# Kernel tuning notes

Measured on AMD Instinct MI355X. Metric: run time of the kernel, lower is better.

## Reference

```python
import jax, jax.numpy as jnp
import numpy as np

N = 50000
E0 = 800000
IN_CH = 128
HID = 64
OUT_CH = 64
HEADS = 2
NEG_SLOPE = 0.2


def _xavier(key, shape):
    fan_in, fan_out = shape[-2], shape[-1]
    limit = (6.0 / (fan_in + fan_out)) ** 0.5
    return jax.random.uniform(key, shape, jnp.float32, -limit, limit)


def setup_inputs() -> dict:
    key = jax.random.key(0)
    ks = jax.random.split(key, 10)
    x = jax.random.normal(ks[0], (N, IN_CH), jnp.float32)
    src = jax.random.randint(ks[1], (E0,), 0, N)
    dst = jax.random.randint(ks[2], (E0,), 0, N)
    dst = jnp.where(src == dst, (dst + 1) % N, dst)  # no self loops in input
    edge_index = jnp.stack([src, dst]).astype(jnp.int64)
    emb_w = _xavier(ks[3], (HID, IN_CH))
    emb_b = jnp.zeros((HID,), jnp.float32)
    # layer 0: in=HID, out=HID, heads=HEADS
    w0 = _xavier(ks[4], (HEADS, HID, HID))
    a0 = _xavier(ks[5], (1, HEADS, 2 * HID))
    # layer 1: in=HEADS*HID, out=HID, heads=HEADS
    w1 = _xavier(ks[6], (HEADS, HEADS * HID, HID))
    a1 = _xavier(ks[7], (1, HEADS, 2 * HID))
    # layer 2: in=HEADS*HID, out=OUT_CH, heads=1, concat=False
    w2 = _xavier(ks[8], (1, HEADS * HID, OUT_CH))
    a2 = _xavier(ks[9], (1, 1, 2 * OUT_CH))
    return {"x": x, "edge_index": edge_index, "emb_w": emb_w, "emb_b": emb_b,
            "w0": w0, "a0": a0, "w1": w1, "a1": a1, "w2": w2, "a2": a2}


def gat_layer(x, w, a, src, dst, concat):
    # x: [N, F_in]; w: [H, F_in, C]; a: [1, H, 2C]; src/dst: [E]
    C = w.shape[-1]
    xh = jnp.einsum('nf,hfc->nhc', x, w)               # [N, H, C]
    a_i, a_j = a[0, :, :C], a[0, :, C:]                # each [H, C]
    # (cat(x_i, x_j) * a).sum(-1) == <x_i, a_i> + <x_j, a_j>; compute per node then gather
    s_i = jnp.einsum('nhc,hc->nh', xh, a_i)            # [N, H]
    s_j = jnp.einsum('nhc,hc->nh', xh, a_j)            # [N, H]
    alpha = jax.nn.leaky_relu(s_i[dst] + s_j[src], NEG_SLOPE)  # [E, H]
    # segment softmax over destination nodes
    m = jax.ops.segment_max(alpha, dst, num_segments=N)
    alpha = jnp.exp(alpha - m[dst])
    denom = jax.ops.segment_sum(alpha, dst, num_segments=N)
    alpha = alpha / (denom[dst] + 1e-16)
    out = jax.ops.segment_sum(xh[src] * alpha[:, :, None], dst, num_segments=N)  # [N, H, C]
    if concat:
        return out.reshape(N, -1)
    return out.mean(axis=1)


def _forward(x, edge_index, emb_w, emb_b, w0, a0, w1, a1, w2, a2):
    # add self loops (inputs contain none, matching remove+add in the source)
    loop = jnp.arange(N, dtype=edge_index.dtype)
    src = jnp.concatenate([edge_index[0], loop])
    dst = jnp.concatenate([edge_index[1], loop])
    h = x @ emb_w.T + emb_b                            # nn.Linear embedding
    h = jax.nn.elu(gat_layer(h, w0, a0, src, dst, True))
    h = jax.nn.elu(gat_layer(h, w1, a1, src, dst, True))
    h = jax.nn.elu(gat_layer(h, w2, a2, src, dst, False))
    return h


def reference(x, edge_index, emb_w, emb_b, w0, a0, w1, a1, w2, a2):
    return _forward(x, edge_index, emb_w, emb_b, w0, a0, w1, a1, w2, a2)
```

## Files before the change

### kernel.cpp

```cpp
#include <hip/hip_runtime.h>
#include <math.h>

typedef __attribute__((ext_vector_type(8))) short short8v;
typedef __attribute__((ext_vector_type(4))) float float4v;

union uf32 { unsigned int u; float f; };

__device__ __forceinline__ unsigned short f2b(float f) {
  uf32 v; v.f = f;
  unsigned int u = v.u;
  return (unsigned short)((u + 0x7fffu + ((u >> 16) & 1u)) >> 16);
}

__global__ void zero8(int* __restrict__ p, int n) {
  int i = blockIdx.x * 256 + threadIdx.x;
  if (i < n) p[i] = 0;
}

__global__ void hist8(const int* __restrict__ ei, int* __restrict__ cnt8,
                      unsigned short* __restrict__ lpos, int E0, int N) {
  int e = blockIdx.x * 256 + threadIdx.x;
  if (e >= E0 + N) return;
  int vx = blockIdx.x & 7;
  int d = (e < E0) ? ei[E0 + e] : (e - E0);
  lpos[e] = (unsigned short)atomicAdd(&cnt8[vx * N + d], 1);
}

__global__ void fold8(const int* __restrict__ cnt8, int* __restrict__ base8,
                      int* __restrict__ cnt, int* __restrict__ part, int N) {
  __shared__ int lds[256];
  int d = blockIdx.x * 256 + threadIdx.x;
  int run = 0;
  if (d < N) {
#pragma unroll
    for (int x = 0; x < 8; ++x) {
      int t = cnt8[x * N + d];
      base8[x * N + d] = run;
      run += t;
    }
    cnt[d] = run;
  }
  lds[threadIdx.x] = (d < N) ? run : 0;
  __syncthreads();
  for (int o = 128; o; o >>= 1) {
    if (threadIdx.x < o) lds[threadIdx.x] += lds[threadIdx.x + o];
    __syncthreads();
  }
  if (threadIdx.x == 0) part[blockIdx.x] = lds[0];
}

__global__ void scan_carry(int* __restrict__ part, int nb) {
  __shared__ int lds[256];
  __shared__ int carry;
  if (threadIdx.x == 0) carry = 0;
  __syncthreads();
  for (int t0 = 0; t0 < nb; t0 += 256) {
    int t = t0 + threadIdx.x;
    int v = (t < nb) ? part[t] : 0;
    lds[threadIdx.x] = v;
    __syncthreads();
    for (int o = 1; o < 256; o <<= 1) {
      int x = (threadIdx.x >= o) ? lds[threadIdx.x - o] : 0;
      __syncthreads();
      lds[threadIdx.x] += x;
      __syncthreads();
    }
    if (t < nb) part[t] = carry + lds[threadIdx.x] - v;
    __syncthreads();
    if (threadIdx.x == 255) carry += lds[255];
    __syncthreads();
  }
}

__global__ void scan3(const int* __restrict__ cnt, const int* __restrict__ part,
                      int* __restrict__ rp, int N, int E) {
  __shared__ int lds[256];
  int t = threadIdx.x;
  int idx = blockIdx.x * 256 + t;
  int v = (idx < N) ? cnt[idx] : 0;
  lds[t] = v;
  __syncthreads();
  for (int o = 1; o < 256; o <<= 1) {
    int x = (t >= o) ? lds[t - o] : 0;
    __syncthreads();
    lds[t] += x;
    __syncthreads();
  }
  if (idx < N) rp[idx] = part[blockIdx.x] + lds[t] - v;
  if (blockIdx.x == 0 && t == 0) rp[N] = E;
}

__global__ void addrp(const int* __restrict__ rp, const int* __restrict__ base8,
                      int* __restrict__ rb8, int N) {
  int d = blockIdx.x * 256 + threadIdx.x;
  int x = blockIdx.y;
  if (d < N) rb8[x * N + d] = rp[d] + base8[x * N + d];
}

__global__ void fillx(const int* __restrict__ ei, const int* __restrict__ rb8,
                      const unsigned short* __restrict__ lpos,
                      int* __restrict__ col, int E0, int N) {
  int e = blockIdx.x * 256 + threadIdx.x;
  if (e >= E0 + N) return;
  int vx = blockIdx.x & 7;
  int s, d;
  if (e < E0) { s = ei[e]; d = ei[E0 + e]; }
  else        { s = e - E0; d = s; }
  col[rb8[vx * N + d] + lpos[e]] = s;
}

__global__ void pack_w(const float* __restrict__ w, unsigned short* __restrict__ bp,
                       int F, int sf, int sc, int hstride) {
  int h = blockIdx.y;
  int i = blockIdx.x * 256 + threadIdx.x;
  if (i >= F * 64) return;
  int j = i & 7, colc = (i >> 3) & 15, g = (i >> 7) & 3, ct = (i >> 9) & 3, kk = i >> 11;
  int f = kk * 32 + g * 8 + j;
  int c = ct * 16 + colc;
  float v = w[(size_t)h * hstride + (size_t)f * sf + (size_t)c * sc];
  bp[(size_t)h * F * 64 + i] = f2b(v);
}

template <int F, int H, bool SCORES, bool BIAS, bool IBF, bool OBF>
__global__ __launch_bounds__(256) void gemm_mfma(
    const void* __restrict__ in, const unsigned short* __restrict__ bp,
    const float* __restrict__ bias, const float* __restrict__ a,
    void* __restrict__ xh_out, float* __restrict__ si, float* __restrict__ sj,
    int nrows) {
  constexpr int SA = F + 8;
  constexpr int NK = F / 32;
  constexpr int HC = H * 64;
  __shared__ __align__(16) unsigned short A_lds[64 * SA];

  const int tid = threadIdx.x;
  const int lane = tid & 63;
  const int wv = tid >> 6;
  const int h = blockIdx.y;
  const int n0 = blockIdx.x * 64;

  if (IBF) {
    const unsigned short* inb = (const unsigned short*)in;
    constexpr int NCH = 64 * F / 8;
#pragma unroll
    for (int i0 = 0; i0 < NCH; i0 += 256) {
      const int i = i0 + tid;
      const int row = i / (F / 8);
      const int c8 = i % (F / 8);
      int rg = n0 + row;
      if (rg >= nrows) rg = nrows - 1;
      const short8v v = *reinterpret_cast<const short8v*>(inb + (size_t)rg * F + c8 * 8);
      *reinterpret_cast<short8v*>(A_lds + row * SA + c8 * 8) = v;
    }
  } else {
    const float* inf = (const float*)in;
    constexpr int NCH = 64 * F / 4;
#pragma unroll
    for (int i0 = 0; i0 < NCH; i0 += 256) {
      const int i = i0 + tid;
      const int row = i / (F / 4);
      const int c4 = i % (F / 4);
      int rg = n0 + row;
      if (rg >= nrows) rg = nrows - 1;
      const float4 v = *reinterpret_cast<const float4*>(inf + (size_t)rg * F + c4 * 4);
      unsigned short* d = A_lds + row * SA + c4 * 4;
      d[0] = f2b(v.x); d[1] = f2b(v.y); d[2] = f2b(v.z); d[3] = f2b(v.w);
    }
  }
  __syncthreads();

  const int g = lane >> 4;
  const int cl = lane & 15;
  const unsigned short* __restrict__ bph = bp + (size_t)h * (NK * 4 * 4 * 128);

  float4v acc[4];
#pragma unroll
  for (int ct = 0; ct < 4; ++ct) acc[ct] = (float4v){0.f, 0.f, 0.f, 0.f};

  const unsigned short* ar = A_lds + (wv * 16 + cl) * SA + g * 8;
#pragma unroll
  for (int kk = 0; kk < NK; ++kk) {
    const short8v af = *reinterpret_cast<const short8v*>(ar + kk * 32);
#pragma unroll
    for (int ct = 0; ct < 4; ++ct) {
      const short8v bf = *reinterpret_cast<const short8v*>(
          bph + ((size_t)((kk * 4 + ct) * 4 + g)) * 128 + cl * 8);
      acc[ct] = __builtin_amdgcn_mfma_f32_16x16x32_bf16(af, bf, acc[ct], 0, 0, 0);
    }
  }

  if (BIAS) {
#pragma unroll
    for (int ct = 0; ct < 4; ++ct) {
      const float b = bias[ct * 16 + cl];
#pragma unroll
      for (int reg = 0; reg < 4; ++reg) acc[ct][reg] += b;
    }
  }

#pragma unroll
  for (int ct = 0; ct < 4; ++ct) {
    const int c = ct * 16 + cl;
#pragma unroll
    for (int reg = 0; reg < 4; ++reg) {
      const int n = n0 + wv * 16 + g * 4 + reg;
      if (n < nrows) {
        const size_t idx = (size_t)n * HC + h * 64 + c;
        if (OBF) ((unsigned short*)xh_out)[idx] = f2b(acc[ct][reg]);
        else     ((float*)xh_out)[idx] = acc[ct][reg];
      }
    }
  }

  if (SCORES) {
    float pi[4] = {0.f, 0.f, 0.f, 0.f}, pj[4] = {0.f, 0.f, 0.f, 0.f};
#pragma unroll
    for (int ct = 0; ct < 4; ++ct) {
      const float av = a[h * 128 + ct * 16 + cl];
      const float bv = a[h * 128 + 64 + ct * 16 + cl];
#pragma unroll
      for (int reg = 0; reg < 4; ++reg) {
        pi[reg] = fmaf(acc[ct][reg], av, pi[reg]);
        pj[reg] = fmaf(acc[ct][reg], bv, pj[reg]);
      }
    }
#pragma unroll
    for (int reg = 0; reg < 4; ++reg) {
#pragma unroll
      for (int o = 8; o; o >>= 1) {
        pi[reg] += __shfl_xor(pi[reg], o, 64);
        pj[reg] += __shfl_xor(pj[reg], o, 64);
      }
    }
    if (cl == 0) {
#pragma unroll
      for (int reg = 0; reg < 4; ++reg) {
        const int n = n0 + wv * 16 + g * 4 + reg;
        if (n < nrows) {
          si[(size_t)n * H + h] = pi[reg];
          sj[(size_t)n * H + h] = pj[reg];
        }
      }
    }
  }
}

template <int H, bool OBF>
__global__ __launch_bounds__(256) void agg_kernel(
    const unsigned short* __restrict__ xh, const float* __restrict__ si_g,
    const float* __restrict__ sj_g, const int* __restrict__ rp,
    const int* __restrict__ col, void* __restrict__ out, int N) {
  constexpr int HC = H * 64;
  const int lane = threadIdx.x & 63;
  const int n = blockIdx.x * 4 + (threadIdx.x >> 6);
  if (n >= N) return;
  const int el = lane & 31;
  const int hl = (H == 2) ? (lane >> 5) : 0;

  const int base = rp[n];
  const int deg = rp[n + 1] - base;
  const float siv = si_g[(size_t)n * H + hl];

  const int soff = (H == 1) ? (lane >> 5) : 0;
  const int qoff = (H == 1) ? (lane >> 5) : (lane & 32);
  constexpr int STEP = (H == 2) ? 1 : 2;
  const unsigned int loff = (H == 2) ? (unsigned)lane * 2 : (unsigned)el * 2;

  float m = -INFINITY, den = 0.f, acc0 = 0.f, acc1 = 0.f;

  for (int start = 0; start < deg; start += 32) {
    const int k = start + el;
    const bool vld = k < deg;
    const int s = vld ? col[base + k] : 0;
    float al = -INFINITY;
    if (vld) {
      const float t = siv + sj_g[(size_t)s * H + hl];
      al = (t > 0.f) ? t : 0.2f * t;
    }
    float cm = al;
#pragma unroll
    for (int o = 16; o; o >>= 1) cm = fmaxf(cm, __shfl_xor(cm, o, 64));
    const float nm = fmaxf(m, cm);
    const float r = __expf(m - nm);
    den *= r; acc0 *= r; acc1 *= r; m = nm;
    const float p = vld ? __expf(al - m) : 0.f;
    float ps = p;
#pragma unroll
    for (int o = 16; o; o >>= 1) ps += __shfl_xor(ps, o, 64);
    den += ps;

    const int cc = min(32, deg - start);
    int kk = 0;
    for (; kk + 4 * STEP <= cc; kk += 4 * STEP) {
      int sb[4]; float qb[4]; unsigned int uv[4];
#pragma unroll
      for (int u = 0; u < 4; ++u) {
        const int e = kk + u * STEP;
        sb[u] = __shfl(s, e + soff, 64);
        qb[u] = __shfl(p, e + qoff, 64);
      }
#pragma unroll
      for (int u = 0; u < 4; ++u)
        uv[u] = *reinterpret_cast<const unsigned int*>(xh + (size_t)sb[u] * HC + loff);
#pragma unroll
      for (int u = 0; u < 4; ++u) {
        uf32 lo, hi;
        lo.u = uv[u] << 16;
        hi.u = uv[u] & 0xffff0000u;
        acc0 = fmaf(qb[u], lo.f, acc0);
        acc1 = fmaf(qb[u], hi.f, acc1);
      }
    }
    for (; kk < cc; kk += STEP) {
      const int sb = __shfl(s, kk + soff, 64);
      const float qb = __shfl(p, kk + qoff, 64);
      const unsigned int uv = *reinterpret_cast<const unsigned int*>(xh + (size_t)sb * HC + loff);
      uf32 lo, hi;
      lo.u = uv << 16;
      hi.u = uv & 0xffff0000u;
      acc0 = fmaf(qb, lo.f, acc0);
      acc1 = fmaf(qb, hi.f, acc1);
    }
  }

  if (H == 2) {
    const float invd = 1.f / (den + 1e-16f);
    float v0 = acc0 * invd, v1 = acc1 * invd;
    v0 = (v0 > 0.f) ? v0 : expm1f(v0);
    v1 = (v1 > 0.f) ? v1 : expm1f(v1);
    if (OBF) {
      unsigned int pk = ((unsigned int)f2b(v1) << 16) | (unsigned int)f2b(v0);
      *reinterpret_cast<unsigned int*>((unsigned short*)out + (size_t)n * 128 + lane * 2) = pk;
    } else {
      float2 o; o.x = v0; o.y = v1;
      *reinterpret_cast<float2*>((float*)out + (size_t)n * 128 + lane * 2) = o;
    }
  } else {
    acc0 += __shfl_xor(acc0, 32, 64);
    acc1 += __shfl_xor(acc1, 32, 64);
    if (lane < 32) {
      const float invd = 1.f / (den + 1e-16f);
      float v0 = acc0 * invd, v1 = acc1 * invd;
      v0 = (v0 > 0.f) ? v0 : expm1f(v0);
      v1 = (v1 > 0.f) ? v1 : expm1f(v1);
      if (OBF) {
        unsigned int pk = ((unsigned int)f2b(v1) << 16) | (unsigned int)f2b(v0);
        *reinterpret_cast<unsigned int*>((unsigned short*)out + (size_t)n * 64 + el * 2) = pk;
      } else {
        float2 o; o.x = v0; o.y = v1;
        *reinterpret_cast<float2*>((float*)out + (size_t)n * 64 + el * 2) = o;
      }
    }
  }
}

extern "C" void kernel_launch(void* const* d_in, const int* in_sizes, int n_in,
                              void* d_out, int out_size, void* d_ws, size_t ws_size,
                              hipStream_t stream) {
  const float* x     = (const float*)d_in[0];
  const int*   ei    = (const int*)d_in[1];
  const float* emb_w = (const float*)d_in[2];
  const float* emb_b = (const float*)d_in[3];
  const float* w0    = (const float*)d_in[4];
  const float* a0    = (const float*)d_in[5];
  const float* w1    = (const float*)d_in[6];
  const float* a1    = (const float*)d_in[7];
  const float* w2    = (const float*)d_in[8];
  const float* a2    = (const float*)d_in[9];

  const int IN_CH = 128;
  int N  = in_sizes[0] / IN_CH;
  int E0 = in_sizes[1] / 2;
  int E  = E0 + N;

  char* p = (char*)d_ws;
  auto alloc = [&](size_t bytes) -> char* {
    char* r = p;
    p += (bytes + 255) & ~(size_t)255;
    return r;
  };
  unsigned short* hA  = (unsigned short*)alloc((size_t)N * 128 * 2);
  unsigned short* hB  = (unsigned short*)alloc((size_t)N * 128 * 2);
  unsigned short* xhb = (unsigned short*)alloc((size_t)N * 128 * 2);
  float* si   = (float*)alloc((size_t)N * 2 * 4);
  float* sj   = (float*)alloc((size_t)N * 2 * 4);
  unsigned short* packE = (unsigned short*)alloc(128 * 64 * 2);
  unsigned short* pack0 = (unsigned short*)alloc(2 * 64 * 64 * 2);
  unsigned short* pack1 = (unsigned short*)alloc(2 * 128 * 64 * 2);
  unsigned short* pack2 = (unsigned short*)alloc(128 * 64 * 2);
  int* rp    = (int*)alloc((size_t)(N + 1) * 4);
  int* cnt   = (int*)alloc((size_t)N * 4);
  int* cnt8  = (int*)alloc((size_t)8 * N * 4);
  int* base8 = (int*)alloc((size_t)8 * N * 4);
  int* rb8   = (int*)alloc((size_t)8 * N * 4);
  unsigned short* lpos = (unsigned short*)alloc((size_t)E * 2);
  int* col   = (int*)alloc((size_t)E * 4);
  int* part  = (int*)alloc(1024);

  dim3 blk(256);
  int gN = (N + 255) / 256;
  int gE = (E + 255) / 256;

  zero8<<<(8 * N + 255) / 256, blk, 0, stream>>>(cnt8, 8 * N);
  hist8<<<gE, blk, 0, stream>>>(ei, cnt8, lpos, E0, N);
  fold8<<<gN, blk, 0, stream>>>(cnt8, base8, cnt, part, N);
  scan_carry<<<1, blk, 0, stream>>>(part, gN);
  scan3<<<gN, blk, 0, stream>>>(cnt, part, rp, N, E);
  addrp<<<dim3(gN, 8), blk, 0, stream>>>(rp, base8, rb8, N);
  fillx<<<gE, blk, 0, stream>>>(ei, rb8, lpos, col, E0, N);

  pack_w<<<dim3(32, 1), blk, 0, stream>>>(emb_w, packE, 128, 1, 128, 0);
  pack_w<<<dim3(16, 2), blk, 0, stream>>>(w0, pack0, 64, 64, 1, 64 * 64);
  pack_w<<<dim3(32, 2), blk, 0, stream>>>(w1, pack1, 128, 64, 1, 128 * 64);
  pack_w<<<dim3(32, 1), blk, 0, stream>>>(w2, pack2, 128, 64, 1, 0);

  int gR = (N + 63) / 64;

  gemm_mfma<128, 1, false, true, false, true><<<dim3(gR, 1), blk, 0, stream>>>(
      x, packE, emb_b, nullptr, hA, nullptr, nullptr, N);

  gemm_mfma<64, 2, true, false, true, true><<<dim3(gR, 2), blk, 0, stream>>>(
      hA, pack0, nullptr, a0, xhb, si, sj, N);
  agg_kernel<2, true><<<(N + 3) / 4, blk, 0, stream>>>(xhb, si, sj, rp, col, hB, N);

  gemm_mfma<128, 2, true, false, true, true><<<dim3(gR, 2), blk, 0, stream>>>(
      hB, pack1, nullptr, a1, xhb, si, sj, N);
  agg_kernel<2, true><<<(N + 3) / 4, blk, 0, stream>>>(xhb, si, sj, rp, col, hA, N);

  gemm_mfma<128, 1, true, false, true, true><<<dim3(gR, 1), blk, 0, stream>>>(
      hA, pack2, nullptr, a2, xhb, si, sj, N);
  agg_kernel<1, false><<<(N + 3) / 4, blk, 0, stream>>>(xhb, si, sj, rp, col, (float*)d_out, N);
}
```

Measured before the change: 215.6 us.

## Fuse setup kernels, loop heads inside GEMM, and widen aggregation unroll

Folds the addrp kernel into scan3 and merges the four pack_w launches into one pack_all launch, cutting the number of kernel launches. The GEMM now loops over heads inside each block, so the A tile is loaded into LDS once instead of once per head, with the A fragments kept in registers. The aggregation kernel skips the rescale step on its first chunk and adds an 8-way unrolled gather loop to keep more loads in flight. The costs are higher register pressure and a grid that is half as large for the two-head GEMMs.

```diff
diff --git a/kernel.cpp b/kernel.cpp
--- a/kernel.cpp
+++ b/kernel.cpp
@@ -73,7 +73,8 @@
 }
 
 __global__ void scan3(const int* __restrict__ cnt, const int* __restrict__ part,
-                      int* __restrict__ rp, int N, int E) {
+                      const int* __restrict__ base8, int* __restrict__ rp,
+                      int* __restrict__ rb8, int N, int E) {
   __shared__ int lds[256];
   int t = threadIdx.x;
   int idx = blockIdx.x * 256 + t;
@@ -86,15 +87,13 @@
     lds[t] += x;
     __syncthreads();
   }
-  if (idx < N) rp[idx] = part[blockIdx.x] + lds[t] - v;
+  if (idx < N) {
+    const int rpv = part[blockIdx.x] + lds[t] - v;
+    rp[idx] = rpv;
+#pragma unroll
+    for (int x = 0; x < 8; ++x) rb8[x * N + idx] = rpv + base8[x * N + idx];
+  }
   if (blockIdx.x == 0 && t == 0) rp[N] = E;
-}
-
-__global__ void addrp(const int* __restrict__ rp, const int* __restrict__ base8,
-                      int* __restrict__ rb8, int N) {
-  int d = blockIdx.x * 256 + threadIdx.x;
-  int x = blockIdx.y;
-  if (d < N) rb8[x * N + d] = rp[d] + base8[x * N + d];
 }
 
 __global__ void fillx(const int* __restrict__ ei, const int* __restrict__ rb8,
@@ -109,15 +108,23 @@
   col[rb8[vx * N + d] + lpos[e]] = s;
 }
 
-__global__ void pack_w(const float* __restrict__ w, unsigned short* __restrict__ bp,
-                       int F, int sf, int sc, int hstride) {
-  int h = blockIdx.y;
-  int i = blockIdx.x * 256 + threadIdx.x;
+__global__ void pack_all(const float* __restrict__ emb_w, const float* __restrict__ w0,
+                         const float* __restrict__ w1, const float* __restrict__ w2,
+                         unsigned short* __restrict__ pE, unsigned short* __restrict__ p0,
+                         unsigned short* __restrict__ p1, unsigned short* __restrict__ p2) {
+  int b = blockIdx.x;
+  const float* w; unsigned short* bp;
+  int F, sf, sc, h;
+  if (b < 32)       { w = emb_w; bp = pE; F = 128; sf = 1;  sc = 128; h = 0; }
+  else if (b < 64)  { b -= 32;  w = w0; bp = p0; F = 64;  sf = 64; sc = 1; h = b / 16; b %= 16; }
+  else if (b < 128) { b -= 64;  w = w1; bp = p1; F = 128; sf = 64; sc = 1; h = b / 32; b %= 32; }
+  else              { b -= 128; w = w2; bp = p2; F = 128; sf = 64; sc = 1; h = 0; }
+  int i = b * 256 + threadIdx.x;
   if (i >= F * 64) return;
   int j = i & 7, colc = (i >> 3) & 15, g = (i >> 7) & 3, ct = (i >> 9) & 3, kk = i >> 11;
   int f = kk * 32 + g * 8 + j;
   int c = ct * 16 + colc;
-  float v = w[(size_t)h * hstride + (size_t)f * sf + (size_t)c * sc];
+  float v = w[(size_t)h * F * 64 + (size_t)f * sf + (size_t)c * sc];
   bp[(size_t)h * F * 64 + i] = f2b(v);
 }
 
@@ -135,7 +142,6 @@
   const int tid = threadIdx.x;
   const int lane = tid & 63;
   const int wv = tid >> 6;
-  const int h = blockIdx.y;
   const int n0 = blockIdx.x * 64;
 
   if (IBF) {
@@ -170,74 +176,81 @@
 
   const int g = lane >> 4;
   const int cl = lane & 15;
-  const unsigned short* __restrict__ bph = bp + (size_t)h * (NK * 4 * 4 * 128);
-
-  float4v acc[4];
-#pragma unroll
-  for (int ct = 0; ct < 4; ++ct) acc[ct] = (float4v){0.f, 0.f, 0.f, 0.f};
-
+
+  short8v af[NK];
   const unsigned short* ar = A_lds + (wv * 16 + cl) * SA + g * 8;
 #pragma unroll
-  for (int kk = 0; kk < NK; ++kk) {
-    const short8v af = *reinterpret_cast<const short8v*>(ar + kk * 32);
+  for (int kk = 0; kk < NK; ++kk) af[kk] = *reinterpret_cast<const short8v*>(ar + kk * 32);
+
+#pragma unroll
+  for (int h = 0; h < H; ++h) {
+    const unsigned short* __restrict__ bph = bp + (size_t)h * (F * 64);
+
+    float4v acc[4];
+#pragma unroll
+    for (int ct = 0; ct < 4; ++ct) acc[ct] = (float4v){0.f, 0.f, 0.f, 0.f};
+
+#pragma unroll
+    for (int kk = 0; kk < NK; ++kk) {
+#pragma unroll
+      for (int ct = 0; ct < 4; ++ct) {
+        const short8v bf = *reinterpret_cast<const short8v*>(
+            bph + ((size_t)((kk * 4 + ct) * 4 + g)) * 128 + cl * 8);
+        acc[ct] = __builtin_amdgcn_mfma_f32_16x16x32_bf16(af[kk], bf, acc[ct], 0, 0, 0);
+      }
+    }
+
+    if (BIAS) {
+#pragma unroll
+      for (int ct = 0; ct < 4; ++ct) {
+        const float b = bias[ct * 16 + cl];
+#pragma unroll
+        for (int reg = 0; reg < 4; ++reg) acc[ct][reg] += b;
+      }
+    }
+
 #pragma unroll
     for (int ct = 0; ct < 4; ++ct) {
-      const short8v bf = *reinterpret_cast<const short8v*>(
-          bph + ((size_t)((kk * 4 + ct) * 4 + g)) * 128 + cl * 8);
-      acc[ct] = __builtin_amdgcn_mfma_f32_16x16x32_bf16(af, bf, acc[ct], 0, 0, 0);
-    }
-  }
-
-  if (BIAS) {
-#pragma unroll
-    for (int ct = 0; ct < 4; ++ct) {
-      const float b = bias[ct * 16 + cl];
-#pragma unroll
-      for (int reg = 0; reg < 4; ++reg) acc[ct][reg] += b;
-    }
-  }
-
-#pragma unroll
-  for (int ct = 0; ct < 4; ++ct) {
-    const int c = ct * 16 + cl;
-#pragma unroll
-    for (int reg = 0; reg < 4; ++reg) {
-      const int n = n0 + wv * 16 + g * 4 + reg;
-      if (n < nrows) {
-        const size_t idx = (size_t)n * HC + h * 64 + c;
-        if (OBF) ((unsigned short*)xh_out)[idx] = f2b(acc[ct][reg]);
-        else     ((float*)xh_out)[idx] = acc[ct][reg];
-      }
-    }
-  }
-
-  if (SCORES) {
-    float pi[4] = {0.f, 0.f, 0.f, 0.f}, pj[4] = {0.f, 0.f, 0.f, 0.f};
-#pragma unroll
-    for (int ct = 0; ct < 4; ++ct) {
-      const float av = a[h * 128 + ct * 16 + cl];
-      const float bv = a[h * 128 + 64 + ct * 16 + cl];
-#pragma unroll
-      for (int reg = 0; reg < 4; ++reg) {
-        pi[reg] = fmaf(acc[ct][reg], av, pi[reg]);
-        pj[reg] = fmaf(acc[ct][reg], bv, pj[reg]);
-      }
-    }
-#pragma unroll
-    for (int reg = 0; reg < 4; ++reg) {
-#pragma unroll
-      for (int o = 8; o; o >>= 1) {
-        pi[reg] += __shfl_xor(pi[reg], o, 64);
-        pj[reg] += __shfl_xor(pj[reg], o, 64);
-      }
-    }
-    if (cl == 0) {
+      const int c = ct * 16 + cl;
 #pragma unroll
       for (int reg = 0; reg < 4; ++reg) {
         const int n = n0 + wv * 16 + g * 4 + reg;
         if (n < nrows) {
-          si[(size_t)n * H + h] = pi[reg];
-          sj[(size_t)n * H + h] = pj[reg];
+          const size_t idx = (size_t)n * HC + h * 64 + c;
+          if (OBF) ((unsigned short*)xh_out)[idx] = f2b(acc[ct][reg]);
+          else     ((float*)xh_out)[idx] = acc[ct][reg];
+        }
+      }
+    }
+
+    if (SCORES) {
+      float pi[4] = {0.f, 0.f, 0.f, 0.f}, pj[4] = {0.f, 0.f, 0.f, 0.f};
+#pragma unroll
+      for (int ct = 0; ct < 4; ++ct) {
+        const float av = a[h * 128 + ct * 16 + cl];
+        const float bv = a[h * 128 + 64 + ct * 16 + cl];
+#pragma unroll
+        for (int reg = 0; reg < 4; ++reg) {
+          pi[reg] = fmaf(acc[ct][reg], av, pi[reg]);
+          pj[reg] = fmaf(acc[ct][reg], bv, pj[reg]);
+        }
+      }
+#pragma unroll
+      for (int reg = 0; reg < 4; ++reg) {
+#pragma unroll
+        for (int o = 8; o; o >>= 1) {
+          pi[reg] += __shfl_xor(pi[reg], o, 64);
+          pj[reg] += __shfl_xor(pj[reg], o, 64);
+        }
+      }
+      if (cl == 0) {
+#pragma unroll
+        for (int reg = 0; reg < 4; ++reg) {
+          const int n = n0 + wv * 16 + g * 4 + reg;
+          if (n < nrows) {
+            si[(size_t)n * H + h] = pi[reg];
+            sj[(size_t)n * H + h] = pj[reg];
+          }
         }
       }
     }
@@ -265,7 +278,7 @@
   constexpr int STEP = (H == 2) ? 1 : 2;
   const unsigned int loff = (H == 2) ? (unsigned)lane * 2 : (unsigned)el * 2;
 
-  float m = -INFINITY, den = 0.f, acc0 = 0.f, acc1 = 0.f;
+  float m = 0.f, den = 0.f, acc0 = 0.f, acc1 = 0.f;
 
   for (int start = 0; start < deg; start += 32) {
     const int k = start + el;
@@ -279,9 +292,13 @@
     float cm = al;
 #pragma unroll
     for (int o = 16; o; o >>= 1) cm = fmaxf(cm, __shfl_xor(cm, o, 64));
-    const float nm = fmaxf(m, cm);
-    const float r = __expf(m - nm);
-    den *= r; acc0 *= r; acc1 *= r; m = nm;
+    if (start == 0) {
+      m = cm;
+    } else {
+      const float nm = fmaxf(m, cm);
+      const float r = __expf(m - nm);
+      den *= r; acc0 *= r; acc1 *= r; m = nm;
+    }
     const float p = vld ? __expf(al - m) : 0.f;
     float ps = p;
 #pragma unroll
@@ -290,6 +307,26 @@
 
     const int cc = min(32, deg - start);
     int kk = 0;
+    for (; kk + 8 * STEP <= cc; kk += 8 * STEP) {
+      int sb[8]; float qb[8]; unsigned int uv[8];
+#pragma unroll
+      for (int u = 0; u < 8; ++u) {
+        const int e = kk + u * STEP;
+        sb[u] = __shfl(s, e + soff, 64);
+        qb[u] = __shfl(p, e + qoff, 64);
+      }
+#pragma unroll
+      for (int u = 0; u < 8; ++u)
+        uv[u] = *reinterpret_cast<const unsigned int*>(xh + (size_t)sb[u] * HC + loff);
+#pragma unroll
+      for (int u = 0; u < 8; ++u) {
+        uf32 lo, hi;
+        lo.u = uv[u] << 16;
+        hi.u = uv[u] & 0xffff0000u;
+        acc0 = fmaf(qb[u], lo.f, acc0);
+        acc1 = fmaf(qb[u], hi.f, acc1);
+      }
+    }
     for (; kk + 4 * STEP <= cc; kk += 4 * STEP) {
       int sb[4]; float qb[4]; unsigned int uv[4];
 #pragma unroll
@@ -404,29 +441,25 @@
   hist8<<<gE, blk, 0, stream>>>(ei, cnt8, lpos, E0, N);
   fold8<<<gN, blk, 0, stream>>>(cnt8, base8, cnt, part, N);
   scan_carry<<<1, blk, 0, stream>>>(part, gN);
-  scan3<<<gN, blk, 0, stream>>>(cnt, part, rp, N, E);
-  addrp<<<dim3(gN, 8), blk, 0, stream>>>(rp, base8, rb8, N);
+  scan3<<<gN, blk, 0, stream>>>(cnt, part, base8, rp, rb8, N, E);
   fillx<<<gE, blk, 0, stream>>>(ei, rb8, lpos, col, E0, N);
 
-  pack_w<<<dim3(32, 1), blk, 0, stream>>>(emb_w, packE, 128, 1, 128, 0);
-  pack_w<<<dim3(16, 2), blk, 0, stream>>>(w0, pack0, 64, 64, 1, 64 * 64);
-  pack_w<<<dim3(32, 2), blk, 0, stream>>>(w1, pack1, 128, 64, 1, 128 * 64);
-  pack_w<<<dim3(32, 1), blk, 0, stream>>>(w2, pack2, 128, 64, 1, 0);
+  pack_all<<<160, blk, 0, stream>>>(emb_w, w0, w1, w2, packE, pack0, pack1, pack2);
 
   int gR = (N + 63) / 64;
 
-  gemm_mfma<128, 1, false, true, false, true><<<dim3(gR, 1), blk, 0, stream>>>(
+  gemm_mfma<128, 1, false, true, false, true><<<gR, blk, 0, stream>>>(
       x, packE, emb_b, nullptr, hA, nullptr, nullptr, N);
 
-  gemm_mfma<64, 2, true, false, true, true><<<dim3(gR, 2), blk, 0, stream>>>(
+  gemm_mfma<64, 2, true, false, true, true><<<gR, blk, 0, stream>>>(
       hA, pack0, nullptr, a0, xhb, si, sj, N);
   agg_kernel<2, true><<<(N + 3) / 4, blk, 0, stream>>>(xhb, si, sj, rp, col, hB, N);
 
-  gemm_mfma<128, 2, true, false, true, true><<<dim3(gR, 2), blk, 0, stream>>>(
+  gemm_mfma<128, 2, true, false, true, true><<<gR, blk, 0, stream>>>(
       hB, pack1, nullptr, a1, xhb, si, sj, N);
   agg_kernel<2, true><<<(N + 3) / 4, blk, 0, stream>>>(xhb, si, sj, rp, col, hA, N);
 
-  gemm_mfma<128, 1, true, false, true, true><<<dim3(gR, 1), blk, 0, stream>>>(
+  gemm_mfma<128, 1, true, false, true, true><<<gR, blk, 0, stream>>>(
       hA, pack2, nullptr, a2, xhb, si, sj, N);
   agg_kernel<1, false><<<(N + 3) / 4, blk, 0, stream>>>(xhb, si, sj, rp, col, (float*)d_out, N);
 }
```

After: 205.7 us. 4.6% less time.
